# Optimization experiments

Hardware: AMD Instinct MI355X
Metric: run time of the kernel (lower is better)

Reference implementation:

```python
import jax, jax.numpy as jnp
import numpy as np

B, N, D = 4, 8192, 1024
H, DK = 8, 128          # d_k = D // H
FF = 4096
EPS = 1e-5


def setup_inputs() -> dict:
    key = jax.random.key(0)
    ks = jax.random.split(key, 8)
    s = 0.02  # init scale for weights
    return {
        "x": jax.random.normal(ks[0], (B, N, D), jnp.float32),
        "delta_x": jax.random.uniform(ks[1], (N,), jnp.float32),
        # Linear weights stored [in, out] (math-equivalent to torch's x @ W.T)
        "Wq": jax.random.normal(ks[2], (D, D), jnp.float32) * s,
        "bq": jnp.zeros((D,), jnp.float32),
        "Wk": jax.random.normal(ks[3], (D, D), jnp.float32) * s,
        "bk": jnp.zeros((D,), jnp.float32),
        "Wv": jax.random.normal(ks[4], (D, D), jnp.float32) * s,
        "bv": jnp.zeros((D,), jnp.float32),
        # per-head LayerNorm params for K; NOTE: the original code (faithfully
        # reproduced) applies layernorms_K to BOTH key and value in Galerkin mode.
        "gamma_k": jnp.ones((H, DK), jnp.float32),
        "beta_k": jnp.zeros((H, DK), jnp.float32),
        "W1": jax.random.normal(ks[5], (D, FF), jnp.float32) * s,
        "b1": jnp.zeros((FF,), jnp.float32),
        "W2": jax.random.normal(ks[6], (FF, D), jnp.float32) * s,
        "b2": jnp.zeros((D,), jnp.float32),
    }


def _per_head_ln(t, gamma, beta):
    # t: [B, H, N, DK]; torch LayerNorm: biased variance over last dim
    mu = jnp.mean(t, axis=-1, keepdims=True)
    var = jnp.mean(jnp.square(t - mu), axis=-1, keepdims=True)
    t = (t - mu) * jax.lax.rsqrt(var + EPS)
    return t * gamma[None, :, None, :] + beta[None, :, None, :]


def reference(x, delta_x, Wq, bq, Wk, bk, Wv, bv, gamma_k, beta_k, W1, b1, W2, b2):
    b, n, d = x.shape

    def heads(y):  # [b, n, d] -> [b, H, n, DK]
        return y.reshape(b, n, H, DK).transpose(0, 2, 1, 3)

    q = heads(x @ Wq + bq)
    k = heads(x @ Wk + bk)
    v = heads(x @ Wv + bv)

    k = _per_head_ln(k, gamma_k, beta_k)
    v = _per_head_ln(v, gamma_k, beta_k)  # layernorms_K reused on value (as in source)
    k = k * delta_x[None, None, :, None]  # einsum('bhxd,x->bhxd')

    # Galerkin (softmax-free, linear) attention: (K^T V) / N then Q @ (.)
    scores = jnp.einsum("bhnd,bhne->bhde", k, v) / n  # [b,H,DK,DK]
    attn_out = jnp.einsum("bhnd,bhde->bhne", q, scores)  # [b,H,n,DK]
    # (F.dropout in the source treated as identity: inference/eval semantics)

    x = x + attn_out.transpose(0, 2, 1, 3).reshape(b, n, d)  # residual 1
    h = jax.nn.silu(x @ W1 + b1)
    return x + (h @ W2 + b2)  # residual 2
```

## Files before the change

kernel.cpp:

```cpp
#include <hip/hip_runtime.h>
#include <hip/hip_bf16.h>
#include <stdint.h>

#define DEV __device__ __forceinline__

typedef __attribute__((ext_vector_type(8))) short bf16x8;
typedef __attribute__((ext_vector_type(8))) unsigned short u16x8;
typedef __attribute__((ext_vector_type(4))) unsigned short u16x4;
typedef __attribute__((ext_vector_type(4))) float f32x4;

static constexpr int BB = 4, NN = 8192, DD = 1024, HH = 8, DKK = 128, FFF = 4096;
static constexpr int MM = BB * NN;

DEV float bfb2f(unsigned int s) { unsigned int x = s << 16; float f; __builtin_memcpy(&f, &x, 4); return f; }
DEV unsigned short f2bfb(float f) {
    unsigned int x; __builtin_memcpy(&x, &f, 4);
    x += 0x7fffu + ((x >> 16) & 1u);
    return (unsigned short)(x >> 16);
}

DEV void gload_lds16(const void* g, void* l) {
    auto gp = (const __attribute__((address_space(1))) void*)(uintptr_t)g;
    auto lp = (__attribute__((address_space(3))) void*)(unsigned int)(uintptr_t)l;
    __builtin_amdgcn_global_load_lds(gp, lp, 16, 0, 0);
}

__global__ void k_pack_bf16(const float* __restrict__ in, unsigned short* __restrict__ ob, long n) {
    long i = ((long)blockIdx.x * blockDim.x + threadIdx.x) * 8;
    if (i >= n) return;
    f32x4 a = *(const f32x4*)&in[i];
    f32x4 b = *(const f32x4*)&in[i + 4];
    u16x8 o;
    o[0]=f2bfb(a[0]); o[1]=f2bfb(a[1]); o[2]=f2bfb(a[2]); o[3]=f2bfb(a[3]);
    o[4]=f2bfb(b[0]); o[5]=f2bfb(b[1]); o[6]=f2bfb(b[2]); o[7]=f2bfb(b[3]);
    *(u16x8*)&ob[i] = o;
}

__global__ void k_transpose(const float* __restrict__ W, unsigned short* __restrict__ WT, int R, int C) {
    __shared__ float t[32][33];
    const int tid = threadIdx.x;
    const int r0 = blockIdx.y * 32, c0 = blockIdx.x * 32;
    const int lr = tid >> 3, lc = (tid & 7) * 4;
    f32x4 v = *(const f32x4*)&W[(long)(r0 + lr) * C + c0 + lc];
    t[lr][lc + 0] = v[0]; t[lr][lc + 1] = v[1]; t[lr][lc + 2] = v[2]; t[lr][lc + 3] = v[3];
    __syncthreads();
    const int oc = tid >> 3, orr = (tid & 7) * 4;
    u16x4 o;
    o[0] = f2bfb(t[orr + 0][oc]); o[1] = f2bfb(t[orr + 1][oc]);
    o[2] = f2bfb(t[orr + 2][oc]); o[3] = f2bfb(t[orr + 3][oc]);
    *(u16x4*)&WT[(long)(c0 + oc) * R + r0 + orr] = o;
}

template <int EPI>
__global__ __launch_bounds__(512, 2)
void k_gemm256(const unsigned short* __restrict__ A, int lda,
               const unsigned short* __restrict__ BT, int ldbt,
               const float* __restrict__ bias0, const float* __restrict__ bias1,
               const float* __restrict__ bias2,
               const unsigned short* __restrict__ resb,
               unsigned short* __restrict__ outp0, unsigned short* __restrict__ outp1,
               unsigned short* __restrict__ outp2,
               float* __restrict__ outf,
               int K, int gridx)
{
    extern __shared__ __align__(128) unsigned short smem[];
    unsigned short* As = smem;
    unsigned short* Bs = smem + 4 * 8192;

    const int nwg = gridDim.x;
    int wg = blockIdx.x;
    {
        const int q = nwg >> 3, r = nwg & 7;
        const int xcd = wg & 7, idx = wg >> 3;
        wg = (xcd < r ? xcd * (q + 1) : r * (q + 1) + (xcd - r) * q) + idx;
    }
    const int brow = (wg / gridx) * 256;
    const int bcol = (wg % gridx) * 256;

    const int tid = threadIdx.x;
    const int lane = tid & 63;
    const int w = tid >> 6;
    const int wm = w >> 2, wn = w & 3;
    const int fr = lane & 15;
    const int kg = lane >> 4;

    const int dl = tid * 16;
    const int soff = dl ^ (((dl >> 7) & 3) << 4);
    const int arow = soff >> 6;
    const int akel = (soff & 63) >> 1;
    const unsigned short* Ab = A + (long)(brow + arow) * lda + akel;
    const unsigned short* Bb = BT + (long)(bcol + arow) * ldbt + akel;

    int aoff[8], boff[4];
    #pragma unroll
    for (int m = 0; m < 8; ++m) { int o = (wm * 128 + m * 16 + fr) * 64 + kg * 16; aoff[m] = o ^ (((o >> 7) & 3) << 4); }
    #pragma unroll
    for (int n = 0; n < 4; ++n) { int o = (wn * 64 + n * 16 + fr) * 64 + kg * 16; boff[n] = o ^ (((o >> 7) & 3) << 4); }

    f32x4 acc[8][4] = {};

#define STG_A(u, ks, slot) do { \
        const unsigned short* _g = Ab + (long)(u) * 64 + (ks) * 32; \
        gload_lds16(_g,              (slot) + tid * 8); \
        gload_lds16(_g + 128L * lda, (slot) + 4096 + tid * 8); } while (0)
#define STG_B(u, ks, slot) do { \
        const unsigned short* _g = Bb + (long)(u) * 64 + (ks) * 32; \
        gload_lds16(_g,               (slot) + tid * 8); \
        gload_lds16(_g + 128L * ldbt, (slot) + 4096 + tid * 8); } while (0)

#define BAR() __builtin_amdgcn_s_barrier()
#define LGKM(N) do { asm volatile("s_waitcnt lgkmcnt(" #N ")" ::: "memory"); \
                     __builtin_amdgcn_sched_barrier(0); } while (0)
#define VM8() asm volatile("s_waitcnt vmcnt(8)" ::: "memory")

#define MFMA16(AF, BF, R0) do { \
        __builtin_amdgcn_s_setprio(1); \
        _Pragma("unroll") \
        for (int m = 0; m < 4; ++m) { \
            _Pragma("unroll") \
            for (int n = 0; n < 4; ++n) \
                acc[(R0) + m][n] = __builtin_amdgcn_mfma_f32_16x16x32_bf16(AF[m], BF[n], acc[(R0) + m][n], 0, 0, 0); \
        } \
        __builtin_amdgcn_s_setprio(0); } while (0)

#define DO_TILE(sa0, sa1, sb0, sb1, STG0, STG1, STG2, STG3) do { \
        bf16x8 b0f[4], a0f[4], a1f[4], b1f[4], a2f[4], a3f[4]; \
         \
        _Pragma("unroll") \
        for (int n = 0; n < 4; ++n) b0f[n] = *(const bf16x8*)((const char*)(sb0) + boff[n]); \
        _Pragma("unroll") \
        for (int m = 0; m < 4; ++m) a0f[m] = *(const bf16x8*)((const char*)(sa0) + aoff[m]); \
        _Pragma("unroll") \
        for (int m = 0; m < 4; ++m) a1f[m] = *(const bf16x8*)((const char*)(sa0) + aoff[m + 4]); \
        STG0; \
        BAR(); LGKM(4); \
        MFMA16(a0f, b0f, 0); \
        BAR(); \
         \
        STG1; VM8(); \
        BAR(); LGKM(0); \
        MFMA16(a1f, b0f, 4); \
        BAR(); \
         \
        _Pragma("unroll") \
        for (int n = 0; n < 4; ++n) b1f[n] = *(const bf16x8*)((const char*)(sb1) + boff[n]); \
        _Pragma("unroll") \
        for (int m = 0; m < 4; ++m) a2f[m] = *(const bf16x8*)((const char*)(sa1) + aoff[m]); \
        _Pragma("unroll") \
        for (int m = 0; m < 4; ++m) a3f[m] = *(const bf16x8*)((const char*)(sa1) + aoff[m + 4]); \
        STG2; \
        BAR(); LGKM(4); \
        MFMA16(a2f, b1f, 0); \
        BAR(); \
         \
        STG3; VM8(); \
        BAR(); LGKM(0); \
        MFMA16(a3f, b1f, 4); \
        BAR(); \
    } while (0)

    unsigned short* A0 = As;            unsigned short* A1 = As + 8192;
    unsigned short* A2 = As + 16384;    unsigned short* A3 = As + 24576;
    unsigned short* B0 = Bs;            unsigned short* B1 = Bs + 8192;
    unsigned short* B2 = Bs + 16384;    unsigned short* B3 = Bs + 24576;

    const int NT = K >> 6;
    STG_A(0, 0, A0); STG_B(0, 0, B0);
    STG_B(0, 1, B1); STG_A(0, 1, A1);
    STG_A(1, 0, A2); STG_B(1, 0, B2);
    VM8();
    BAR();

    for (int t = 0; t < NT; t += 2) {
        const int u1 = t + 1;
        const int u2 = (t + 2 < NT) ? t + 2 : 0;
        const int u3 = (t + 3 < NT) ? t + 3 : 0;
        DO_TILE(A0, A1, B0, B1,
                STG_B(u1, 1, B3), STG_A(u1, 1, A3), STG_A(u2, 0, A0), STG_B(u2, 0, B0));
        DO_TILE(A2, A3, B2, B3,
                STG_B(u2, 1, B1), STG_A(u2, 1, A1), STG_A(u3, 0, A2), STG_B(u3, 0, B2));
    }
    asm volatile("s_waitcnt vmcnt(0)" ::: "memory");
#undef DO_TILE
#undef MFMA16
#undef VM8
#undef LGKM
#undef BAR
#undef STG_A
#undef STG_B

    const int q4 = (lane >> 4) * 4;
    if constexpr (EPI == 1) {
        const int mat = bcol >> 10;
        const float* bp = mat == 0 ? bias0 : (mat == 1 ? bias1 : bias2);
        unsigned short* op = mat == 0 ? outp0 : (mat == 1 ? outp1 : outp2);
        const int dc0 = bcol & 1023;
        #pragma unroll
        for (int m = 0; m < 8; ++m)
            #pragma unroll
            for (int n = 0; n < 4; ++n) {
                const int c = dc0 + wn * 64 + n * 16 + fr;
                const float bv = bp[c];
                const int hh = c >> 7, dk = c & 127;
                #pragma unroll
                for (int j = 0; j < 4; ++j) {
                    const int r = brow + wm * 128 + m * 16 + q4 + j;
                    const long idx = (((long)(r >> 13) * 8 + hh) * 8192 + (r & 8191)) * 128 + dk;
                    op[idx] = f2bfb(acc[m][n][j] + bv);
                }
            }
    } else if constexpr (EPI == 2) {
        #pragma unroll
        for (int m = 0; m < 8; ++m)
            #pragma unroll
            for (int n = 0; n < 4; ++n) {
                const int c = bcol + wn * 64 + n * 16 + fr;
                const float bv = bias0[c];
                #pragma unroll
                for (int j = 0; j < 4; ++j) {
                    const int r = brow + wm * 128 + m * 16 + q4 + j;
                    float v = acc[m][n][j] + bv;
                    v = v / (1.f + __expf(-v));
                    outp0[(long)r * FFF + c] = f2bfb(v);
                }
            }
    } else {
        #pragma unroll
        for (int m = 0; m < 8; ++m)
            #pragma unroll
            for (int n = 0; n < 4; ++n) {
                const int c = bcol + wn * 64 + n * 16 + fr;
                const float bv = bias0[c];
                #pragma unroll
                for (int j = 0; j < 4; ++j) {
                    const int r = brow + wm * 128 + m * 16 + q4 + j;
                    float v = acc[m][n][j] + bv + bfb2f(resb[(long)r * DD + c]);
                    outf[(long)r * DD + c] = v;
                }
            }
    }
}

template <int EPI>
__global__ __launch_bounds__(256, 2)
void k_gemm(const unsigned short* __restrict__ A, int lda, long sAz,
            const unsigned short* __restrict__ BT, int ldbt, long sBz,
            const float* __restrict__ bias,
            const float* __restrict__ resf,
            const unsigned short* __restrict__ resb,
            unsigned short* __restrict__ outp,
            float* __restrict__ outf,
            int K)
{
    __shared__ __align__(16) unsigned short As[128 * 32];
    __shared__ __align__(16) unsigned short Bs[128 * 32];
    const int tid = threadIdx.x;
    const int z = blockIdx.z;
    A  += (long)z * sAz;
    BT += (long)z * sBz;
    const int brow = blockIdx.y * 128;
    const int bcol = blockIdx.x * 128;

    const int c0 = tid, c1 = tid + 256;
    const unsigned short* Ap0 = A + (long)(brow + (c0 >> 2)) * lda + (c0 & 3) * 8;
    const unsigned short* Ap1 = A + (long)(brow + (c1 >> 2)) * lda + (c1 & 3) * 8;
    const unsigned short* Bp0 = BT + (long)(bcol + (c0 >> 2)) * ldbt + (c0 & 3) * 8;
    const unsigned short* Bp1 = BT + (long)(bcol + (c1 >> 2)) * ldbt + (c1 & 3) * 8;
    unsigned short* AsD0 = &As[c0 * 8];
    unsigned short* AsD1 = &As[c1 * 8];
    unsigned short* BsD0 = &Bs[c0 * 8];
    unsigned short* BsD1 = &Bs[c1 * 8];

    const int lane = tid & 63;
    const int w = tid >> 6;
    const int wr = (w >> 1) * 64;
    const int wc = (w & 1) * 64;
    const int fr = lane & 15;
    const int fk = (lane >> 4) * 8;

    f32x4 acc[4][4] = {};

    for (int kt = 0; kt < K; kt += 32) {
        gload_lds16(Ap0 + kt, AsD0);
        gload_lds16(Ap1 + kt, AsD1);
        gload_lds16(Bp0 + kt, BsD0);
        gload_lds16(Bp1 + kt, BsD1);
        __syncthreads();
        bf16x8 af[4], bfr[4];
        #pragma unroll
        for (int m = 0; m < 4; ++m) af[m] = *(const bf16x8*)&As[(wr + m * 16 + fr) * 32 + fk];
        #pragma unroll
        for (int n = 0; n < 4; ++n) bfr[n] = *(const bf16x8*)&Bs[(wc + n * 16 + fr) * 32 + fk];
        #pragma unroll
        for (int m = 0; m < 4; ++m)
            #pragma unroll
            for (int n = 0; n < 4; ++n)
                acc[m][n] = __builtin_amdgcn_mfma_f32_16x16x32_bf16(af[m], bfr[n], acc[m][n], 0, 0, 0);
        __syncthreads();
    }

    const int orow = (lane >> 4) * 4;
    #pragma unroll
    for (int m = 0; m < 4; ++m) {
        #pragma unroll
        for (int n = 0; n < 4; ++n) {
            const int d = bcol + wc + n * 16 + fr;
            #pragma unroll
            for (int j = 0; j < 4; ++j) {
                const int r = brow + wr + m * 16 + orow + j;
                float v = acc[m][n][j];
                if constexpr (EPI == 3) {
                    long xi = ((long)(z >> 3) * NN + r) * DD + (z & 7) * DKK + d;
                    v += resf[xi];
                    outp[xi] = f2bfb(v);
                }
            }
        }
    }
    (void)bias; (void)resb; (void)outf;
}

__global__ void k_ln(unsigned short* __restrict__ Kb, unsigned short* __restrict__ Vb,
                     const float* __restrict__ gk, const float* __restrict__ bek,
                     const float* __restrict__ dx)
{
    const int tid = threadIdx.x;
    const int lane = tid & 63;
    const long row = (long)blockIdx.x * 4 + (tid >> 6);
    unsigned short* buf = blockIdx.y ? Vb : Kb;
    const int h = (int)((row >> 13) & 7);
    const int n = (int)(row & 8191);
    unsigned int* p = (unsigned int*)(buf + row * 128) + lane;
    const unsigned int u = *p;
    float f0 = bfb2f(u & 0xffffu);
    float f1 = bfb2f(u >> 16);
    float s = f0 + f1, q = f0 * f0 + f1 * f1;
    #pragma unroll
    for (int o = 32; o; o >>= 1) { s += __shfl_xor(s, o); q += __shfl_xor(q, o); }
    const float mean = s * (1.f / 128.f);
    const float var  = q * (1.f / 128.f) - mean * mean;
    const float rstd = rsqrtf(var + 1e-5f);
    const int gi = h * 128 + lane * 2;
    float o0 = (f0 - mean) * rstd * gk[gi]     + bek[gi];
    float o1 = (f1 - mean) * rstd * gk[gi + 1] + bek[gi + 1];
    if (blockIdx.y == 0) { const float dl = dx[n]; o0 *= dl; o1 *= dl; }
    *p = (unsigned int)f2bfb(o0) | ((unsigned int)f2bfb(o1) << 16);
}

__global__ __launch_bounds__(256, 2)
void k_scorespart(const unsigned short* __restrict__ Kb, const unsigned short* __restrict__ Vb,
                  float* __restrict__ part)
{
    __shared__ __align__(16) unsigned short KT[128 * 136];
    __shared__ __align__(16) unsigned short VT[128 * 136];
    const int tid = threadIdx.x;
    const int bh = blockIdx.y, split = blockIdx.x;
    const unsigned short* Kp = Kb + (long)bh * NN * DKK;
    const unsigned short* Vp = Vb + (long)bh * NN * DKK;
    const int lane = tid & 63, w = tid >> 6;
    const int wr = (w >> 1) * 64, wc = (w & 1) * 64, fr = lane & 15, fk = (lane >> 4) * 8;
    const int nrow = tid >> 1, dblk = (tid & 1) * 64;
    f32x4 acc[4][4] = {};
    for (int c = 0; c < 8; ++c) {
        const int n0 = (split * 8 + c) * 128;
        bf16x8 kv[8], vv[8];
        #pragma unroll
        for (int i = 0; i < 8; ++i) {
            kv[i] = *(const bf16x8*)&Kp[(long)(n0 + nrow) * DKK + dblk + i * 8];
            vv[i] = *(const bf16x8*)&Vp[(long)(n0 + nrow) * DKK + dblk + i * 8];
        }
        __syncthreads();
        #pragma unroll
        for (int i = 0; i < 8; ++i)
            #pragma unroll
            for (int j = 0; j < 8; ++j) {
                const int dd = dblk + i * 8 + j;
                KT[dd * 136 + nrow] = (unsigned short)kv[i][j];
                VT[dd * 136 + nrow] = (unsigned short)vv[i][j];
            }
        __syncthreads();
        #pragma unroll
        for (int ks = 0; ks < 4; ++ks) {
            bf16x8 af[4], bfr[4];
            #pragma unroll
            for (int m = 0; m < 4; ++m) af[m] = *(const bf16x8*)&KT[(wr + m * 16 + fr) * 136 + ks * 32 + fk];
            #pragma unroll
            for (int n = 0; n < 4; ++n) bfr[n] = *(const bf16x8*)&VT[(wc + n * 16 + fr) * 136 + ks * 32 + fk];
            #pragma unroll
            for (int m = 0; m < 4; ++m)
                #pragma unroll
                for (int n = 0; n < 4; ++n)
                    acc[m][n] = __builtin_amdgcn_mfma_f32_16x16x32_bf16(af[m], bfr[n], acc[m][n], 0, 0, 0);
        }
    }
    float* P = part + (long)(bh * 8 + split) * 16384;
    const int orow = (lane >> 4) * 4;
    #pragma unroll
    for (int m = 0; m < 4; ++m)
        #pragma unroll
        for (int n = 0; n < 4; ++n)
            #pragma unroll
            for (int j = 0; j < 4; ++j) {
                const int dD = wr + m * 16 + orow + j;
                const int e  = wc + n * 16 + fr;
                P[dD * 128 + e] = acc[m][n][j];
            }
}

__global__ void k_scoresred(const float* __restrict__ part, unsigned short* __restrict__ scT)
{
    const int bh = blockIdx.x, tid = threadIdx.x;
    const float* P = part + (long)bh * 8 * 16384;
    for (int i = tid; i < 16384; i += 256) {
        float s = 0.f;
        #pragma unroll
        for (int sp = 0; sp < 8; ++sp) s += P[sp * 16384 + i];
        const int d = i >> 7, e = i & 127;
        scT[(long)bh * 16384 + e * 128 + d] = f2bfb(s * (1.f / 8192.f));
    }
}

extern "C" void kernel_launch(void* const* d_in, const int* in_sizes, int n_in,
                              void* d_out, int out_size, void* d_ws, size_t ws_size,
                              hipStream_t stream)
{
    const float* x   = (const float*)d_in[0];
    const float* dx  = (const float*)d_in[1];
    const float* Wq  = (const float*)d_in[2];
    const float* bq  = (const float*)d_in[3];
    const float* Wk  = (const float*)d_in[4];
    const float* bk  = (const float*)d_in[5];
    const float* Wv  = (const float*)d_in[6];
    const float* bv  = (const float*)d_in[7];
    const float* gk  = (const float*)d_in[8];
    const float* bek = (const float*)d_in[9];
    const float* W1  = (const float*)d_in[10];
    const float* b1  = (const float*)d_in[11];
    const float* W2  = (const float*)d_in[12];
    const float* b2  = (const float*)d_in[13];
    float* out = (float*)d_out;
    (void)in_sizes; (void)n_in; (void)out_size; (void)ws_size;

    hipFuncSetAttribute((const void*)k_gemm256<1>, hipFuncAttributeMaxDynamicSharedMemorySize, 131072);
    hipFuncSetAttribute((const void*)k_gemm256<2>, hipFuncAttributeMaxDynamicSharedMemorySize, 131072);
    hipFuncSetAttribute((const void*)k_gemm256<3>, hipFuncAttributeMaxDynamicSharedMemorySize, 131072);

    char* ws = (char*)d_ws;
    size_t off = 0;
    auto alloc = [&](size_t bytes) { void* p = ws + off; off += (bytes + 255) & ~(size_t)255; return p; };
    unsigned short* WqkvT = (unsigned short*)alloc((size_t)3 * DD * DD * 2);
    unsigned short* W1T   = (unsigned short*)alloc((size_t)FFF * DD * 2);
    unsigned short* W2T   = (unsigned short*)alloc((size_t)DD * FFF * 2);
    unsigned short* scT   = (unsigned short*)alloc((size_t)32 * 16384 * 2);
    unsigned short* xb    = (unsigned short*)alloc((size_t)MM * DD * 2);
    unsigned short* Kb    = (unsigned short*)alloc((size_t)MM * DD * 2);
    unsigned short* Vb    = (unsigned short*)alloc((size_t)MM * DD * 2);
    unsigned short* x1b   = (unsigned short*)alloc((size_t)MM * DD * 2);
    unsigned short* hb    = xb;
    float* part           = (float*)x1b;
    unsigned short* Qb    = (unsigned short*)out;

    k_pack_bf16<<<dim3(((long)MM * DD) / 8 / 256), 256, 0, stream>>>(x, xb, (long)MM * DD);
    k_transpose<<<dim3(DD / 32, DD / 32), 256, 0, stream>>>(Wq, WqkvT, DD, DD);
    k_transpose<<<dim3(DD / 32, DD / 32), 256, 0, stream>>>(Wk, WqkvT + (size_t)DD * DD, DD, DD);
    k_transpose<<<dim3(DD / 32, DD / 32), 256, 0, stream>>>(Wv, WqkvT + (size_t)2 * DD * DD, DD, DD);
    k_transpose<<<dim3(FFF / 32, DD / 32), 256, 0, stream>>>(W1, W1T, DD, FFF);
    k_transpose<<<dim3(DD / 32, FFF / 32), 256, 0, stream>>>(W2, W2T, FFF, DD);

    k_gemm256<1><<<dim3((MM / 256) * (3072 / 256)), 512, 131072, stream>>>(
        xb, DD, WqkvT, DD, bq, bk, bv, nullptr, Qb, Kb, Vb, nullptr, DD, 3072 / 256);

    k_ln<<<dim3((BB * HH * NN) / 4, 2), 256, 0, stream>>>(Kb, Vb, gk, bek, dx);

    k_scorespart<<<dim3(8, 32), 256, 0, stream>>>(Kb, Vb, part);
    k_scoresred<<<dim3(32), 256, 0, stream>>>(part, scT);

    k_gemm<3><<<dim3(1, NN / 128, BB * HH), 256, 0, stream>>>(Qb, DKK, (long)NN * DKK, scT, DKK, 16384L,
                                                              nullptr, x, nullptr, x1b, nullptr, DKK);

    for (int c = 0; c < 2; ++c) {
        const unsigned short* xc = x1b + (size_t)c * 16384 * DD;
        k_gemm256<2><<<dim3((16384 / 256) * (FFF / 256)), 512, 131072, stream>>>(
            xc, DD, W1T, DD, b1, nullptr, nullptr, nullptr, hb, nullptr, nullptr, nullptr, DD, FFF / 256);
        k_gemm256<3><<<dim3((16384 / 256) * (DD / 256)), 512, 131072, stream>>>(
            hb, FFF, W2T, FFF, b2, nullptr, nullptr, xc, nullptr, nullptr, nullptr,
            out + (size_t)c * 16384 * DD, FFF, DD / 256);
    }
}
```

Baseline: 1.035 ms.

## Make 256-tile GEMM persistent with cross-tile prefetch of next tile's operands

Converts the 256x256 GEMM kernel into a persistent kernel launched with 256 workgroups, each looping over several output tiles (npass). The first k-slices of the next tile are staged into LDS during the last k-iterations of the current tile, so the load prologue overlaps with compute and the epilogue. This removes per-tile launch and pipeline fill costs, but replaces the XCD-aware tile remap with a fixed mapping and assumes the grid size equals tiles divided by npass.

Measured after the change: 1.000 ms. 1.03x faster.

```diff
diff --git a/kernel.cpp b/kernel.cpp
--- a/kernel.cpp
+++ b/kernel.cpp
@@ -61,21 +61,13 @@
                unsigned short* __restrict__ outp0, unsigned short* __restrict__ outp1,
                unsigned short* __restrict__ outp2,
                float* __restrict__ outf,
-               int K, int gridx)
+               int K, int gridx, int npass)
 {
     extern __shared__ __align__(128) unsigned short smem[];
     unsigned short* As = smem;
     unsigned short* Bs = smem + 4 * 8192;
 
-    const int nwg = gridDim.x;
-    int wg = blockIdx.x;
-    {
-        const int q = nwg >> 3, r = nwg & 7;
-        const int xcd = wg & 7, idx = wg >> 3;
-        wg = (xcd < r ? xcd * (q + 1) : r * (q + 1) + (xcd - r) * q) + idx;
-    }
-    const int brow = (wg / gridx) * 256;
-    const int bcol = (wg % gridx) * 256;
+    const int wg0 = (blockIdx.x & 7) * 32 + (blockIdx.x >> 3);
 
     const int tid = threadIdx.x;
     const int lane = tid & 63;
@@ -88,8 +80,6 @@
     const int soff = dl ^ (((dl >> 7) & 3) << 4);
     const int arow = soff >> 6;
     const int akel = (soff & 63) >> 1;
-    const unsigned short* Ab = A + (long)(brow + arow) * lda + akel;
-    const unsigned short* Bb = BT + (long)(bcol + arow) * ldbt + akel;
 
     int aoff[8], boff[4];
     #pragma unroll
@@ -97,14 +87,12 @@
     #pragma unroll
     for (int n = 0; n < 4; ++n) { int o = (wn * 64 + n * 16 + fr) * 64 + kg * 16; boff[n] = o ^ (((o >> 7) & 3) << 4); }
 
-    f32x4 acc[8][4] = {};
-
-#define STG_A(u, ks, slot) do { \
-        const unsigned short* _g = Ab + (long)(u) * 64 + (ks) * 32; \
+#define STG_A(base, u, ks, slot) do { \
+        const unsigned short* _g = (base) + (long)(u) * 64 + (ks) * 32; \
         gload_lds16(_g,              (slot) + tid * 8); \
         gload_lds16(_g + 128L * lda, (slot) + 4096 + tid * 8); } while (0)
-#define STG_B(u, ks, slot) do { \
-        const unsigned short* _g = Bb + (long)(u) * 64 + (ks) * 32; \
+#define STG_B(base, u, ks, slot) do { \
+        const unsigned short* _g = (base) + (long)(u) * 64 + (ks) * 32; \
         gload_lds16(_g,               (slot) + tid * 8); \
         gload_lds16(_g + 128L * ldbt, (slot) + 4096 + tid * 8); } while (0)
 
@@ -125,7 +113,6 @@
 
 #define DO_TILE(sa0, sa1, sb0, sb1, STG0, STG1, STG2, STG3) do { \
         bf16x8 b0f[4], a0f[4], a1f[4], b1f[4], a2f[4], a3f[4]; \
-         \
         _Pragma("unroll") \
         for (int n = 0; n < 4; ++n) b0f[n] = *(const bf16x8*)((const char*)(sb0) + boff[n]); \
         _Pragma("unroll") \
@@ -136,12 +123,10 @@
         BAR(); LGKM(4); \
         MFMA16(a0f, b0f, 0); \
         BAR(); \
-         \
         STG1; VM8(); \
         BAR(); LGKM(0); \
         MFMA16(a1f, b0f, 4); \
         BAR(); \
-         \
         _Pragma("unroll") \
         for (int n = 0; n < 4; ++n) b1f[n] = *(const bf16x8*)((const char*)(sb1) + boff[n]); \
         _Pragma("unroll") \
@@ -152,7 +137,6 @@
         BAR(); LGKM(4); \
         MFMA16(a2f, b1f, 0); \
         BAR(); \
-         \
         STG3; VM8(); \
         BAR(); LGKM(0); \
         MFMA16(a3f, b1f, 4); \
@@ -165,20 +149,94 @@
     unsigned short* B2 = Bs + 16384;    unsigned short* B3 = Bs + 24576;
 
     const int NT = K >> 6;
-    STG_A(0, 0, A0); STG_B(0, 0, B0);
-    STG_B(0, 1, B1); STG_A(0, 1, A1);
-    STG_A(1, 0, A2); STG_B(1, 0, B2);
+
+    int wg = wg0;
+    int brow = (wg / gridx) * 256;
+    int bcol = (wg % gridx) * 256;
+    const unsigned short* Ab = A + (long)(brow + arow) * lda + akel;
+    const unsigned short* Bb = BT + (long)(bcol + arow) * ldbt + akel;
+    STG_A(Ab, 0, 0, A0); STG_B(Bb, 0, 0, B0);
+    STG_B(Bb, 0, 1, B1); STG_A(Ab, 0, 1, A1);
+    STG_A(Ab, 1, 0, A2); STG_B(Bb, 1, 0, B2);
     VM8();
     BAR();
 
-    for (int t = 0; t < NT; t += 2) {
-        const int u1 = t + 1;
-        const int u2 = (t + 2 < NT) ? t + 2 : 0;
-        const int u3 = (t + 3 < NT) ? t + 3 : 0;
+    for (int p = 0; p < npass; ++p) {
+        const int wgN = (p + 1 < npass) ? (wg0 + (p + 1) * 256) : wg0;
+        const int browN = (wgN / gridx) * 256;
+        const int bcolN = (wgN % gridx) * 256;
+        const unsigned short* Ab2 = A + (long)(browN + arow) * lda + akel;
+        const unsigned short* Bb2 = BT + (long)(bcolN + arow) * ldbt + akel;
+
+        f32x4 acc[8][4] = {};
+
+        for (int t = 0; t + 2 < NT; t += 2) {
+            DO_TILE(A0, A1, B0, B1,
+                    STG_B(Bb, t + 1, 1, B3), STG_A(Ab, t + 1, 1, A3),
+                    STG_A(Ab, t + 2, 0, A0), STG_B(Bb, t + 2, 0, B0));
+            DO_TILE(A2, A3, B2, B3,
+                    STG_B(Bb, t + 2, 1, B1), STG_A(Ab, t + 2, 1, A1),
+                    STG_A(Ab, t + 3, 0, A2), STG_B(Bb, t + 3, 0, B2));
+        }
         DO_TILE(A0, A1, B0, B1,
-                STG_B(u1, 1, B3), STG_A(u1, 1, A3), STG_A(u2, 0, A0), STG_B(u2, 0, B0));
+                STG_B(Bb, NT - 1, 1, B3), STG_A(Ab, NT - 1, 1, A3),
+                STG_A(Ab2, 0, 0, A0), STG_B(Bb2, 0, 0, B0));
         DO_TILE(A2, A3, B2, B3,
-                STG_B(u2, 1, B1), STG_A(u2, 1, A1), STG_A(u3, 0, A2), STG_B(u3, 0, B2));
+                STG_B(Bb2, 0, 1, B1), STG_A(Ab2, 0, 1, A1),
+                STG_A(Ab2, 1, 0, A2), STG_B(Bb2, 1, 0, B2));
+
+        const int q4 = (lane >> 4) * 4;
+        if constexpr (EPI == 1) {
+            const int mat = bcol >> 10;
+            const float* bp = mat == 0 ? bias0 : (mat == 1 ? bias1 : bias2);
+            unsigned short* op = mat == 0 ? outp0 : (mat == 1 ? outp1 : outp2);
+            const int dc0 = bcol & 1023;
+            #pragma unroll
+            for (int m = 0; m < 8; ++m)
+                #pragma unroll
+                for (int n = 0; n < 4; ++n) {
+                    const int c = dc0 + wn * 64 + n * 16 + fr;
+                    const float bv = bp[c];
+                    const int hh = c >> 7, dk = c & 127;
+                    #pragma unroll
+                    for (int j = 0; j < 4; ++j) {
+                        const int r = brow + wm * 128 + m * 16 + q4 + j;
+                        const long idx = (((long)(r >> 13) * 8 + hh) * 8192 + (r & 8191)) * 128 + dk;
+                        op[idx] = f2bfb(acc[m][n][j] + bv);
+                    }
+                }
+        } else if constexpr (EPI == 2) {
+            #pragma unroll
+            for (int m = 0; m < 8; ++m)
+                #pragma unroll
+                for (int n = 0; n < 4; ++n) {
+                    const int c = bcol + wn * 64 + n * 16 + fr;
+                    const float bv = bias0[c];
+                    #pragma unroll
+                    for (int j = 0; j < 4; ++j) {
+                        const int r = brow + wm * 128 + m * 16 + q4 + j;
+                        float v = acc[m][n][j] + bv;
+                        v = v / (1.f + __expf(-v));
+                        outp0[(long)r * FFF + c] = f2bfb(v);
+                    }
+                }
+        } else {
+            #pragma unroll
+            for (int m = 0; m < 8; ++m)
+                #pragma unroll
+                for (int n = 0; n < 4; ++n) {
+                    const int c = bcol + wn * 64 + n * 16 + fr;
+                    const float bv = bias0[c];
+                    #pragma unroll
+                    for (int j = 0; j < 4; ++j) {
+                        const int r = brow + wm * 128 + m * 16 + q4 + j;
+                        float v = acc[m][n][j] + bv + bfb2f(resb[(long)r * DD + c]);
+                        outf[(long)r * DD + c] = v;
+                    }
+                }
+        }
+
+        brow = browN; bcol = bcolN; Ab = Ab2; Bb = Bb2;
     }
     asm volatile("s_waitcnt vmcnt(0)" ::: "memory");
 #undef DO_TILE
@@ -188,57 +246,6 @@
 #undef BAR
 #undef STG_A
 #undef STG_B
-
-    const int q4 = (lane >> 4) * 4;
-    if constexpr (EPI == 1) {
-        const int mat = bcol >> 10;
-        const float* bp = mat == 0 ? bias0 : (mat == 1 ? bias1 : bias2);
-        unsigned short* op = mat == 0 ? outp0 : (mat == 1 ? outp1 : outp2);
-        const int dc0 = bcol & 1023;
-        #pragma unroll
-        for (int m = 0; m < 8; ++m)
-            #pragma unroll
-            for (int n = 0; n < 4; ++n) {
-                const int c = dc0 + wn * 64 + n * 16 + fr;
-                const float bv = bp[c];
-                const int hh = c >> 7, dk = c & 127;
-                #pragma unroll
-                for (int j = 0; j < 4; ++j) {
-                    const int r = brow + wm * 128 + m * 16 + q4 + j;
-                    const long idx = (((long)(r >> 13) * 8 + hh) * 8192 + (r & 8191)) * 128 + dk;
-                    op[idx] = f2bfb(acc[m][n][j] + bv);
-                }
-            }
-    } else if constexpr (EPI == 2) {
-        #pragma unroll
-        for (int m = 0; m < 8; ++m)
-            #pragma unroll
-            for (int n = 0; n < 4; ++n) {
-                const int c = bcol + wn * 64 + n * 16 + fr;
-                const float bv = bias0[c];
-                #pragma unroll
-                for (int j = 0; j < 4; ++j) {
-                    const int r = brow + wm * 128 + m * 16 + q4 + j;
-                    float v = acc[m][n][j] + bv;
-                    v = v / (1.f + __expf(-v));
-                    outp0[(long)r * FFF + c] = f2bfb(v);
-                }
-            }
-    } else {
-        #pragma unroll
-        for (int m = 0; m < 8; ++m)
-            #pragma unroll
-            for (int n = 0; n < 4; ++n) {
-                const int c = bcol + wn * 64 + n * 16 + fr;
-                const float bv = bias0[c];
-                #pragma unroll
-                for (int j = 0; j < 4; ++j) {
-                    const int r = brow + wm * 128 + m * 16 + q4 + j;
-                    float v = acc[m][n][j] + bv + bfb2f(resb[(long)r * DD + c]);
-                    outf[(long)r * DD + c] = v;
-                }
-            }
-    }
 }
 
 template <int EPI>
@@ -467,8 +474,8 @@
     k_transpose<<<dim3(FFF / 32, DD / 32), 256, 0, stream>>>(W1, W1T, DD, FFF);
     k_transpose<<<dim3(DD / 32, FFF / 32), 256, 0, stream>>>(W2, W2T, FFF, DD);
 
-    k_gemm256<1><<<dim3((MM / 256) * (3072 / 256)), 512, 131072, stream>>>(
-        xb, DD, WqkvT, DD, bq, bk, bv, nullptr, Qb, Kb, Vb, nullptr, DD, 3072 / 256);
+    k_gemm256<1><<<dim3(256), 512, 131072, stream>>>(
+        xb, DD, WqkvT, DD, bq, bk, bv, nullptr, Qb, Kb, Vb, nullptr, DD, 3072 / 256, 6);
 
     k_ln<<<dim3((BB * HH * NN) / 4, 2), 256, 0, stream>>>(Kb, Vb, gk, bek, dx);
 
@@ -480,10 +487,10 @@
 
     for (int c = 0; c < 2; ++c) {
         const unsigned short* xc = x1b + (size_t)c * 16384 * DD;
-        k_gemm256<2><<<dim3((16384 / 256) * (FFF / 256)), 512, 131072, stream>>>(
-            xc, DD, W1T, DD, b1, nullptr, nullptr, nullptr, hb, nullptr, nullptr, nullptr, DD, FFF / 256);
-        k_gemm256<3><<<dim3((16384 / 256) * (DD / 256)), 512, 131072, stream>>>(
+        k_gemm256<2><<<dim3(256), 512, 131072, stream>>>(
+            xc, DD, W1T, DD, b1, nullptr, nullptr, nullptr, hb, nullptr, nullptr, nullptr, DD, FFF / 256, 4);
+        k_gemm256<3><<<dim3(256), 512, 131072, stream>>>(
             hb, FFF, W2T, FFF, b2, nullptr, nullptr, xc, nullptr, nullptr, nullptr,
-            out + (size_t)c * 16384 * DD, FFF, DD / 256);
-    }
-}
+            out + (size_t)c * 16384 * DD, FFF, DD / 256, 1);
+    }
+}
```
